# Performance work log

Measured on AMD Instinct MI355X. Metric: run time of the kernel, lower is better.

The kernel has to match this reference:

```python
import jax, jax.numpy as jnp
import numpy as np

K = 16            # top-k negatives kept per row
TEMP = 0.01       # softmax temperature
V = 0.95          # geometric decay base
NEG_FILL = -1e9   # masks out same-class entries before topk (never selected since k << #negatives)


def _l2norm(x):
    # torch F.normalize: x / max(||x||, eps)
    n = jnp.linalg.norm(x, axis=-1, keepdims=True)
    return x / jnp.maximum(n, 1e-12)


def setup_inputs() -> dict:
    key = jax.random.key(0)
    k1, k2, k3 = jax.random.split(key, 3)
    feature = jax.random.normal(k1, (4096, 128), dtype=jnp.float32)
    negative_features = jax.random.normal(k2, (4, 4096, 128), dtype=jnp.float32)
    target = jax.random.randint(k3, (4096,), 0, 4)
    return {"feature": feature, "target": target,
            "negative_features": negative_features, "idx": 0}


def reference(feature, target, negative_features, idx):
    J = negative_features.shape[0]
    f = _l2norm(feature)                       # [n, d]
    negs = _l2norm(negative_features)          # [J, n, d]
    # cosine similarity for every negative set: [J, n, n]
    sims = jnp.einsum('nd,jmd->jnm', f, negs)
    # same-class mask, applied only to the idx-th set
    same = target[:, None] == target[None, :]  # [n, n]
    sims = sims.at[idx].set(jnp.where(same, NEG_FILL, sims[idx]))
    # per-row top-k over the last (candidate) dim: [J, n, K]
    top, _ = jax.lax.top_k(sims, K)
    logits = jnp.transpose(top, (1, 0, 2)) / TEMP   # [n, J, K]
    p = jax.nn.softmax(logits, axis=1)
    logp = jax.nn.log_softmax(logits, axis=1)
    ent = jnp.sum(p * logp, axis=1)                 # [n, K]
    decay = V ** jnp.arange(K, dtype=jnp.float32)
    decay = decay / jnp.sum(decay)                  # L1-normalized, matches F.normalize(p=1)
    loss = jnp.mean(jnp.sum(ent * decay, axis=1)) + jnp.log(jnp.float32(J))
    return loss
```

## Files before the change

kernel.cpp:

```cpp
#include <hip/hip_runtime.h>
#include <hip/hip_bf16.h>
#include <math.h>

#define N 4096
#define D 128
#define NJ 4
#define KTOP 16
#define CSPLIT 2

typedef __attribute__((ext_vector_type(8))) short bf16x8;
typedef __attribute__((ext_vector_type(4))) float f32x4;


__device__ __forceinline__ void ce_desc(float* a, int i, int l) {
    float x = a[i], y = a[l];
    a[i] = fmaxf(x, y);
    a[l] = fminf(x, y);
}

__device__ __forceinline__ void sort16_desc(float* a) {
    ce_desc(a,0,1);  ce_desc(a,2,3);  ce_desc(a,0,2);  ce_desc(a,1,3);  ce_desc(a,1,2);
    ce_desc(a,4,5);  ce_desc(a,6,7);  ce_desc(a,4,6);  ce_desc(a,5,7);  ce_desc(a,5,6);
    ce_desc(a,0,4);  ce_desc(a,2,6);  ce_desc(a,2,4);  ce_desc(a,1,5);  ce_desc(a,3,7);
    ce_desc(a,3,5);  ce_desc(a,1,2);  ce_desc(a,3,4);  ce_desc(a,5,6);
    ce_desc(a,8,9);  ce_desc(a,10,11); ce_desc(a,8,10); ce_desc(a,9,11); ce_desc(a,9,10);
    ce_desc(a,12,13); ce_desc(a,14,15); ce_desc(a,12,14); ce_desc(a,13,15); ce_desc(a,13,14);
    ce_desc(a,8,12); ce_desc(a,10,14); ce_desc(a,10,12); ce_desc(a,9,13); ce_desc(a,11,15);
    ce_desc(a,11,13); ce_desc(a,9,10); ce_desc(a,11,12); ce_desc(a,13,14);
    ce_desc(a,0,8);  ce_desc(a,4,12); ce_desc(a,4,8);  ce_desc(a,2,10); ce_desc(a,6,14);
    ce_desc(a,6,10); ce_desc(a,2,4);  ce_desc(a,6,8);  ce_desc(a,10,12);
    ce_desc(a,1,9);  ce_desc(a,5,13); ce_desc(a,5,9);  ce_desc(a,3,11); ce_desc(a,7,15);
    ce_desc(a,7,11); ce_desc(a,3,5);  ce_desc(a,7,9);  ce_desc(a,11,13);
    ce_desc(a,1,2);  ce_desc(a,3,4);  ce_desc(a,5,6);  ce_desc(a,7,8);  ce_desc(a,9,10);
    ce_desc(a,11,12); ce_desc(a,13,14);
}

__device__ __forceinline__ void bitonic_clean16_desc(float* a) {
    #pragma unroll
    for (int jj = 8; jj > 0; jj >>= 1) {
        #pragma unroll
        for (int i = 0; i < 16; i++) {
            int l = i ^ jj;
            if (l > i) {
                float x = a[i], y = a[l];
                a[i] = fmaxf(x, y);
                a[l] = fminf(x, y);
            }
        }
    }
}

__global__ __launch_bounds__(256) void neguni_prep(
    const float* __restrict__ feat, const float* __restrict__ negs,
    unsigned short* __restrict__ fh, unsigned short* __restrict__ gh)
{
    const int w    = threadIdx.x >> 6;
    const int lane = threadIdx.x & 63;
    const int p    = lane & 15;
    const int rr   = lane >> 4;
    const int row  = blockIdx.x * 16 + w * 4 + rr;

    const float* src = (row < N) ? (feat + (size_t)row * D)
                                 : (negs + (size_t)(row - N) * D);
    float4 v0 = ((const float4*)src)[p * 2];
    float4 v1 = ((const float4*)src)[p * 2 + 1];
    float ss = v0.x*v0.x + v0.y*v0.y + v0.z*v0.z + v0.w*v0.w
             + v1.x*v1.x + v1.y*v1.y + v1.z*v1.z + v1.w*v1.w;
    ss += __shfl_xor(ss, 1, 64);
    ss += __shfl_xor(ss, 2, 64);
    ss += __shfl_xor(ss, 4, 64);
    ss += __shfl_xor(ss, 8, 64);
    const float inv = 1.0f / fmaxf(sqrtf(ss), 1e-12f);

    float f[8] = {v0.x, v0.y, v0.z, v0.w, v1.x, v1.y, v1.z, v1.w};
    unsigned int u[4];
    #pragma unroll
    for (int i = 0; i < 4; i++) {
        __hip_bfloat16 b0 = __float2bfloat16(f[2*i]   * inv);
        __hip_bfloat16 b1 = __float2bfloat16(f[2*i+1] * inv);
        u[i] = ((unsigned int)*(unsigned short*)&b1 << 16) | *(unsigned short*)&b0;
    }
    uint4 pk; pk.x = u[0]; pk.y = u[1]; pk.z = u[2]; pk.w = u[3];

    if (row < N) {
        *(uint4*)(fh + (size_t)row * D + p * 8) = pk;
    } else {
        const int rn  = row - N;
        const int j   = rn >> 12;
        const int rj  = rn & 4095;
        const int chg = rj >> 6;
        const int cl  = rj & 63;
        const int t   = cl >> 4;
        const int col = cl & 15;
        const int s   = p >> 2;
        const int q   = p & 3;
        *(uint4*)(gh + (size_t)j * N * D + (size_t)chg * 8192
                  + (s * 4 + t) * 512 + (q * 16 + col) * 8) = pk;
    }
}

__global__ __launch_bounds__(256) void neguni_main(
    const unsigned short* __restrict__ fh, const unsigned short* __restrict__ gh,
    const int* __restrict__ target, const int* __restrict__ idxp,
    float* __restrict__ topbuf)
{
    __shared__ float tops[4][16][17];

    const int tid   = threadIdx.x;
    const int w     = tid >> 6;
    const int lane  = tid & 63;
    const int col16 = lane & 15;
    const int quad  = lane >> 4;

    const int j   = blockIdx.x & 3;
    const int ft  = (blockIdx.x >> 2) & 255;
    const int cs  = blockIdx.x >> 10;
    const int r0  = ft * 16;
    const int c0  = cs * 2048 + w * 512;
    const int idx = idxp[0];
    const bool msk = (j == idx);

    bf16x8 bfr[4];
    {
        const unsigned short* fr = fh + (size_t)(r0 + col16) * D + quad * 8;
        bfr[0] = *(const bf16x8*)(fr);
        bfr[1] = *(const bf16x8*)(fr + 32);
        bfr[2] = *(const bf16x8*)(fr + 64);
        bfr[3] = *(const bf16x8*)(fr + 96);
    }
    const int rtg = target[r0 + col16];

    const int chg0 = cs * 32 + w * 8;
    const unsigned short* ab0 = gh + (size_t)j * N * D + (size_t)chg0 * 8192 + lane * 8;

    float lst[KTOP];
    f32x4 acc[4];

    {
        bf16x8 fA[16];
        #pragma unroll
        for (int u = 0; u < 16; u++) fA[u] = *(const bf16x8*)(ab0 + u * 512);
        #pragma unroll
        for (int t = 0; t < 4; t++) acc[t] = (f32x4){0.f, 0.f, 0.f, 0.f};
        #pragma unroll
        for (int s = 0; s < 4; s++) {
            #pragma unroll
            for (int t = 0; t < 4; t++)
                acc[t] = __builtin_amdgcn_mfma_f32_16x16x32_bf16(fA[s * 4 + t], bfr[s], acc[t], 0, 0, 0);
        }
    }

    #pragma unroll 1
    for (int ch = 0; ch < 7; ch++) {
        bf16x8 fB[16];
        {
            const unsigned short* ab = ab0 + (size_t)(ch + 1) * 8192;
            #pragma unroll
            for (int u = 0; u < 16; u++) fB[u] = *(const bf16x8*)(ab + u * 512);
        }
        __builtin_amdgcn_sched_barrier(0);

        const int cbase = c0 + ch * 64;
        float s16[16];
        #pragma unroll
        for (int t = 0; t < 4; t++) {
            s16[t * 4 + 0] = acc[t][0];
            s16[t * 4 + 1] = acc[t][1];
            s16[t * 4 + 2] = acc[t][2];
            s16[t * 4 + 3] = acc[t][3];
        }
        if (msk) {
            #pragma unroll
            for (int t = 0; t < 4; t++) {
                int4 tc = *(const int4*)(target + cbase + t * 16 + quad * 4);
                if (tc.x == rtg) s16[t * 4 + 0] = -1e9f;
                if (tc.y == rtg) s16[t * 4 + 1] = -1e9f;
                if (tc.z == rtg) s16[t * 4 + 2] = -1e9f;
                if (tc.w == rtg) s16[t * 4 + 3] = -1e9f;
            }
        }

        sort16_desc(s16);
        if (ch == 0) {
            #pragma unroll
            for (int i = 0; i < 16; i++) lst[i] = s16[i];
        } else {
            float mg[16];
            #pragma unroll
            for (int i = 0; i < 16; i++) mg[i] = fmaxf(lst[i], s16[15 - i]);
            bitonic_clean16_desc(mg);
            #pragma unroll
            for (int i = 0; i < 16; i++) lst[i] = mg[i];
        }

        #pragma unroll
        for (int t = 0; t < 4; t++) acc[t] = (f32x4){0.f, 0.f, 0.f, 0.f};
        #pragma unroll
        for (int s = 0; s < 4; s++) {
            #pragma unroll
            for (int t = 0; t < 4; t++)
                acc[t] = __builtin_amdgcn_mfma_f32_16x16x32_bf16(fB[s * 4 + t], bfr[s], acc[t], 0, 0, 0);
        }
    }

    {
        const int cbase = c0 + 7 * 64;
        float s16[16];
        #pragma unroll
        for (int t = 0; t < 4; t++) {
            s16[t * 4 + 0] = acc[t][0];
            s16[t * 4 + 1] = acc[t][1];
            s16[t * 4 + 2] = acc[t][2];
            s16[t * 4 + 3] = acc[t][3];
        }
        if (msk) {
            #pragma unroll
            for (int t = 0; t < 4; t++) {
                int4 tc = *(const int4*)(target + cbase + t * 16 + quad * 4);
                if (tc.x == rtg) s16[t * 4 + 0] = -1e9f;
                if (tc.y == rtg) s16[t * 4 + 1] = -1e9f;
                if (tc.z == rtg) s16[t * 4 + 2] = -1e9f;
                if (tc.w == rtg) s16[t * 4 + 3] = -1e9f;
            }
        }
        sort16_desc(s16);
        float mg[16];
        #pragma unroll
        for (int i = 0; i < 16; i++) mg[i] = fmaxf(lst[i], s16[15 - i]);
        bitonic_clean16_desc(mg);
        #pragma unroll
        for (int i = 0; i < 16; i++) lst[i] = mg[i];
    }

    #pragma unroll
    for (int off = 16; off <= 32; off <<= 1) {
        float mg[16];
        #pragma unroll
        for (int i = 0; i < 16; i++)
            mg[i] = fmaxf(lst[i], __shfl_xor(lst[15 - i], off, 64));
        bitonic_clean16_desc(mg);
        #pragma unroll
        for (int i = 0; i < 16; i++) lst[i] = mg[i];
    }

    if (lane < 16) {
        #pragma unroll
        for (int i = 0; i < 16; i++) tops[w][lane][i] = lst[i];
        tops[w][lane][16] = -3.0e38f;
    }
    __syncthreads();

    if (tid < 16) {
        int i0 = 0, i1 = 0, i2 = 0, i3 = 0;
        float* outp = topbuf + (((size_t)j * N + r0 + tid) * CSPLIT + cs) * KTOP;
        #pragma unroll
        for (int k = 0; k < KTOP; k++) {
            float v0 = tops[0][tid][i0], v1 = tops[1][tid][i1];
            float v2 = tops[2][tid][i2], v3 = tops[3][tid][i3];
            float m01 = fmaxf(v0, v1), m23 = fmaxf(v2, v3);
            float mx  = fmaxf(m01, m23);
            if      (mx == v0) i0++;
            else if (mx == v1) i1++;
            else if (mx == v2) i2++;
            else               i3++;
            outp[k] = mx;
        }
    }
}

__global__ __launch_bounds__(64) void neguni_fin(
    const float* __restrict__ topbuf, float* __restrict__ out)
{
    __shared__ float buf[64][35];
    __shared__ float mm[16][65];

    const int t     = threadIdx.x;
    const int j     = t >> 4;
    const int row_l = t & 15;
    const int row   = blockIdx.x * 16 + row_l;

    const float4* src = (const float4*)(topbuf + ((size_t)j * N + row) * (CSPLIT * KTOP));
    #pragma unroll
    for (int q = 0; q < 8; q++) {
        float4 v = src[q];
        const int base = (q >> 2) * 17 + (q & 3) * 4;
        buf[t][base + 0] = v.x;
        buf[t][base + 1] = v.y;
        buf[t][base + 2] = v.z;
        buf[t][base + 3] = v.w;
    }
    buf[t][16] = -3.0e38f;
    buf[t][33] = -3.0e38f;

    {
        int ia = 0, ib = 17;
        #pragma unroll
        for (int k = 0; k < KTOP; k++) {
            float va = buf[t][ia], vb = buf[t][ib];
            bool ta = va >= vb;
            mm[row_l][k * 4 + j] = ta ? va : vb;
            if (ta) ia++; else ib++;
        }
    }
    __syncthreads();

    float val = 0.f;
    #pragma unroll
    for (int i = 0; i < 4; i++) {
        const int idx2 = t + i * 64;
        const int rl   = idx2 & 15;
        const int k    = idx2 >> 4;
        float l0 = mm[rl][k * 4 + 0] * 100.0f;
        float l1 = mm[rl][k * 4 + 1] * 100.0f;
        float l2 = mm[rl][k * 4 + 2] * 100.0f;
        float l3 = mm[rl][k * 4 + 3] * 100.0f;
        float m  = fmaxf(fmaxf(l0, l1), fmaxf(l2, l3));
        float d0 = l0 - m, d1 = l1 - m, d2 = l2 - m, d3 = l3 - m;
        float e0 = __expf(d0), e1 = __expf(d1), e2 = __expf(d2), e3 = __expf(d3);
        float s  = e0 + e1 + e2 + e3;
        float ent = (e0 * d0 + e1 * d1 + e2 * d2 + e3 * d3) / s - __logf(s);
        float dk  = __expf(-0.05129329439f * (float)k);
        val += ent * dk;
    }
    val *= (1.0f / (11.1974666f * (float)N));

    #pragma unroll
    for (int off = 32; off > 0; off >>= 1) val += __shfl_xor(val, off, 64);
    if (t == 0) {
        atomicAdd(out, val);
        if (blockIdx.x == 0) atomicAdd(out, 1.38629436112f);
    }
}

extern "C" void kernel_launch(void* const* d_in, const int* in_sizes, int n_in,
                              void* d_out, int out_size, void* d_ws, size_t ws_size,
                              hipStream_t stream) {
    const float* feat   = (const float*)d_in[0];
    const int*   target = (const int*)d_in[1];
    const float* negs   = (const float*)d_in[2];
    const int*   idxp   = (const int*)d_in[3];
    float* out = (float*)d_out;

    unsigned short* fh = (unsigned short*)d_ws;
    unsigned short* gh = fh + (size_t)N * D;
    float* topbuf      = (float*)(gh + (size_t)NJ * N * D);

    hipMemsetAsync(out, 0, sizeof(float), stream);
    neguni_prep<<<dim3((N + NJ * N) / 16), dim3(256), 0, stream>>>(feat, negs, fh, gh);
    neguni_main<<<dim3(NJ * (N / 16) * CSPLIT), dim3(256), 0, stream>>>(fh, gh, target, idxp, topbuf);
    neguni_fin<<<dim3(N / 16), dim3(64), 0, stream>>>(topbuf, out);
}
```

Before: 141.6 us.

## Stage negative-tile repacking through LDS, fold memset into prep, simplify main loop

```diff
diff --git a/kernel.cpp b/kernel.cpp
--- a/kernel.cpp
+++ b/kernel.cpp
@@ -52,54 +52,94 @@
 
 __global__ __launch_bounds__(256) void neguni_prep(
     const float* __restrict__ feat, const float* __restrict__ negs,
-    unsigned short* __restrict__ fh, unsigned short* __restrict__ gh)
+    unsigned short* __restrict__ fh, unsigned short* __restrict__ gh,
+    float* __restrict__ out)
 {
-    const int w    = threadIdx.x >> 6;
-    const int lane = threadIdx.x & 63;
-    const int p    = lane & 15;
-    const int rr   = lane >> 4;
-    const int row  = blockIdx.x * 16 + w * 4 + rr;
-
-    const float* src = (row < N) ? (feat + (size_t)row * D)
-                                 : (negs + (size_t)(row - N) * D);
-    float4 v0 = ((const float4*)src)[p * 2];
-    float4 v1 = ((const float4*)src)[p * 2 + 1];
-    float ss = v0.x*v0.x + v0.y*v0.y + v0.z*v0.z + v0.w*v0.w
-             + v1.x*v1.x + v1.y*v1.y + v1.z*v1.z + v1.w*v1.w;
-    ss += __shfl_xor(ss, 1, 64);
-    ss += __shfl_xor(ss, 2, 64);
-    ss += __shfl_xor(ss, 4, 64);
-    ss += __shfl_xor(ss, 8, 64);
-    const float inv = 1.0f / fmaxf(sqrtf(ss), 1e-12f);
-
-    float f[8] = {v0.x, v0.y, v0.z, v0.w, v1.x, v1.y, v1.z, v1.w};
-    unsigned int u[4];
-    #pragma unroll
-    for (int i = 0; i < 4; i++) {
-        __hip_bfloat16 b0 = __float2bfloat16(f[2*i]   * inv);
-        __hip_bfloat16 b1 = __float2bfloat16(f[2*i+1] * inv);
-        u[i] = ((unsigned int)*(unsigned short*)&b1 << 16) | *(unsigned short*)&b0;
-    }
-    uint4 pk; pk.x = u[0]; pk.y = u[1]; pk.z = u[2]; pk.w = u[3];
-
-    if (row < N) {
+    __shared__ unsigned short lbuf[8192];
+
+    if (blockIdx.x == 0 && threadIdx.x == 0) *out = 0.f;
+
+    if (blockIdx.x < 256) {
+        const int w    = threadIdx.x >> 6;
+        const int lane = threadIdx.x & 63;
+        const int p    = lane & 15;
+        const int rr   = lane >> 4;
+        const int row  = blockIdx.x * 16 + w * 4 + rr;
+
+        const float* src = feat + (size_t)row * D;
+        float4 v0 = ((const float4*)src)[p * 2];
+        float4 v1 = ((const float4*)src)[p * 2 + 1];
+        float ss = v0.x*v0.x + v0.y*v0.y + v0.z*v0.z + v0.w*v0.w
+                 + v1.x*v1.x + v1.y*v1.y + v1.z*v1.z + v1.w*v1.w;
+        ss += __shfl_xor(ss, 1, 64);
+        ss += __shfl_xor(ss, 2, 64);
+        ss += __shfl_xor(ss, 4, 64);
+        ss += __shfl_xor(ss, 8, 64);
+        const float inv = 1.0f / fmaxf(sqrtf(ss), 1e-12f);
+
+        float f[8] = {v0.x, v0.y, v0.z, v0.w, v1.x, v1.y, v1.z, v1.w};
+        unsigned int u[4];
+        #pragma unroll
+        for (int i = 0; i < 4; i++) {
+            __hip_bfloat16 b0 = __float2bfloat16(f[2*i]   * inv);
+            __hip_bfloat16 b1 = __float2bfloat16(f[2*i+1] * inv);
+            u[i] = ((unsigned int)*(unsigned short*)&b1 << 16) | *(unsigned short*)&b0;
+        }
+        uint4 pk; pk.x = u[0]; pk.y = u[1]; pk.z = u[2]; pk.w = u[3];
         *(uint4*)(fh + (size_t)row * D + p * 8) = pk;
     } else {
-        const int rn  = row - N;
-        const int j   = rn >> 12;
-        const int rj  = rn & 4095;
-        const int chg = rj >> 6;
-        const int cl  = rj & 63;
-        const int t   = cl >> 4;
-        const int col = cl & 15;
-        const int s   = p >> 2;
-        const int q   = p & 3;
-        *(uint4*)(gh + (size_t)j * N * D + (size_t)chg * 8192
-                  + (s * 4 + t) * 512 + (q * 16 + col) * 8) = pk;
-    }
-}
-
-__global__ __launch_bounds__(256) void neguni_main(
+        const int c   = blockIdx.x - 256;
+        const int j   = c >> 6;
+        const int chg = c & 63;
+        const int t   = threadIdx.x;
+        const int lr  = t >> 2;
+        const int p4  = t & 3;
+
+        const float* src = negs + ((size_t)(j * 4096 + chg * 64 + lr)) * D + p4 * 32;
+        float4 v[8];
+        float ss = 0.f;
+        #pragma unroll
+        for (int i = 0; i < 8; i++) {
+            v[i] = ((const float4*)src)[i];
+            ss += v[i].x*v[i].x + v[i].y*v[i].y + v[i].z*v[i].z + v[i].w*v[i].w;
+        }
+        ss += __shfl_xor(ss, 1, 64);
+        ss += __shfl_xor(ss, 2, 64);
+        const float inv = 1.0f / fmaxf(sqrtf(ss), 1e-12f);
+
+        float f[32];
+        #pragma unroll
+        for (int i = 0; i < 8; i++) {
+            f[4*i]   = v[i].x; f[4*i+1] = v[i].y;
+            f[4*i+2] = v[i].z; f[4*i+3] = v[i].w;
+        }
+
+        const int t16 = lr >> 4;
+        const int col = lr & 15;
+        #pragma unroll
+        for (int qq = 0; qq < 4; qq++) {
+            unsigned int uu[4];
+            #pragma unroll
+            for (int h = 0; h < 4; h++) {
+                __hip_bfloat16 b0 = __float2bfloat16(f[qq*8 + 2*h]     * inv);
+                __hip_bfloat16 b1 = __float2bfloat16(f[qq*8 + 2*h + 1] * inv);
+                uu[h] = ((unsigned int)*(unsigned short*)&b1 << 16) | *(unsigned short*)&b0;
+            }
+            uint4 pk; pk.x = uu[0]; pk.y = uu[1]; pk.z = uu[2]; pk.w = uu[3];
+            *(uint4*)(lbuf + (p4 * 4 + t16) * 512 + (qq * 16 + col) * 8) = pk;
+        }
+        __syncthreads();
+
+        uint4* dst = (uint4*)(gh + (size_t)j * N * D + (size_t)chg * 8192);
+        const uint4* sb = (const uint4*)lbuf;
+        dst[t]       = sb[t];
+        dst[t + 256] = sb[t + 256];
+        dst[t + 512] = sb[t + 512];
+        dst[t + 768] = sb[t + 768];
+    }
+}
+
+__global__ __launch_bounds__(256, 4) void neguni_main(
     const unsigned short* __restrict__ fh, const unsigned short* __restrict__ gh,
     const int* __restrict__ target, const int* __restrict__ idxp,
     float* __restrict__ topbuf)
@@ -130,35 +170,27 @@
     }
     const int rtg = target[r0 + col16];
 
+    float lst[KTOP];
+
     const int chg0 = cs * 32 + w * 8;
     const unsigned short* ab0 = gh + (size_t)j * N * D + (size_t)chg0 * 8192 + lane * 8;
 
-    float lst[KTOP];
-    f32x4 acc[4];
-
-    {
-        bf16x8 fA[16];
-        #pragma unroll
-        for (int u = 0; u < 16; u++) fA[u] = *(const bf16x8*)(ab0 + u * 512);
+    #pragma unroll 1
+    for (int ch = 0; ch < 8; ch++) {
+        const unsigned short* ab = ab0 + (size_t)ch * 8192;
+
+        f32x4 acc[4];
         #pragma unroll
         for (int t = 0; t < 4; t++) acc[t] = (f32x4){0.f, 0.f, 0.f, 0.f};
+
         #pragma unroll
         for (int s = 0; s < 4; s++) {
             #pragma unroll
-            for (int t = 0; t < 4; t++)
-                acc[t] = __builtin_amdgcn_mfma_f32_16x16x32_bf16(fA[s * 4 + t], bfr[s], acc[t], 0, 0, 0);
-        }
-    }
-
-    #pragma unroll 1
-    for (int ch = 0; ch < 7; ch++) {
-        bf16x8 fB[16];
-        {
-            const unsigned short* ab = ab0 + (size_t)(ch + 1) * 8192;
-            #pragma unroll
-            for (int u = 0; u < 16; u++) fB[u] = *(const bf16x8*)(ab + u * 512);
-        }
-        __builtin_amdgcn_sched_barrier(0);
+            for (int t = 0; t < 4; t++) {
+                bf16x8 a = *(const bf16x8*)(ab + (s * 4 + t) * 512);
+                acc[t] = __builtin_amdgcn_mfma_f32_16x16x32_bf16(a, bfr[s], acc[t], 0, 0, 0);
+            }
+        }
 
         const int cbase = c0 + ch * 64;
         float s16[16];
@@ -192,44 +224,6 @@
             #pragma unroll
             for (int i = 0; i < 16; i++) lst[i] = mg[i];
         }
-
-        #pragma unroll
-        for (int t = 0; t < 4; t++) acc[t] = (f32x4){0.f, 0.f, 0.f, 0.f};
-        #pragma unroll
-        for (int s = 0; s < 4; s++) {
-            #pragma unroll
-            for (int t = 0; t < 4; t++)
-                acc[t] = __builtin_amdgcn_mfma_f32_16x16x32_bf16(fB[s * 4 + t], bfr[s], acc[t], 0, 0, 0);
-        }
-    }
-
-    {
-        const int cbase = c0 + 7 * 64;
-        float s16[16];
-        #pragma unroll
-        for (int t = 0; t < 4; t++) {
-            s16[t * 4 + 0] = acc[t][0];
-            s16[t * 4 + 1] = acc[t][1];
-            s16[t * 4 + 2] = acc[t][2];
-            s16[t * 4 + 3] = acc[t][3];
-        }
-        if (msk) {
-            #pragma unroll
-            for (int t = 0; t < 4; t++) {
-                int4 tc = *(const int4*)(target + cbase + t * 16 + quad * 4);
-                if (tc.x == rtg) s16[t * 4 + 0] = -1e9f;
-                if (tc.y == rtg) s16[t * 4 + 1] = -1e9f;
-                if (tc.z == rtg) s16[t * 4 + 2] = -1e9f;
-                if (tc.w == rtg) s16[t * 4 + 3] = -1e9f;
-            }
-        }
-        sort16_desc(s16);
-        float mg[16];
-        #pragma unroll
-        for (int i = 0; i < 16; i++) mg[i] = fmaxf(lst[i], s16[15 - i]);
-        bitonic_clean16_desc(mg);
-        #pragma unroll
-        for (int i = 0; i < 16; i++) lst[i] = mg[i];
     }
 
     #pragma unroll
@@ -345,8 +339,7 @@
     unsigned short* gh = fh + (size_t)N * D;
     float* topbuf      = (float*)(gh + (size_t)NJ * N * D);
 
-    hipMemsetAsync(out, 0, sizeof(float), stream);
-    neguni_prep<<<dim3((N + NJ * N) / 16), dim3(256), 0, stream>>>(feat, negs, fh, gh);
+    neguni_prep<<<dim3(512), dim3(256), 0, stream>>>(feat, negs, fh, gh, out);
     neguni_main<<<dim3(NJ * (N / 16) * CSPLIT), dim3(256), 0, stream>>>(fh, gh, target, idxp, topbuf);
     neguni_fin<<<dim3(N / 16), dim3(64), 0, stream>>>(topbuf, out);
 }
```

Result: faster. 134.2 us (-5.2%).
